# Kernel tuning notes

Measured on AMD Instinct MI355X. Metric: run time of the kernel, lower is better.

The kernel has to match this reference:

```python
import jax, jax.numpy as jnp
import numpy as np
from jax import lax

K_SQ = 8  # scaling-and-squaring steps (GridExp default)


def lrelu(x):
    return jnp.where(x >= 0, x, 0.2 * x)


def conv(x, w, b, stride=1):
    y = lax.conv_general_dilated(x, w, (stride,) * 3, 'SAME',
                                 dimension_numbers=('NCDHW', 'OIDHW', 'NCDHW'))
    return y + b[None, :, None, None, None]


def convt(x, w, b):
    y = lax.conv_transpose(x, w, (2, 2, 2), 'SAME',
                           dimension_numbers=('NCDHW', 'OIDHW', 'NCDHW'))
    return y + b[None, :, None, None, None]


def identity_grid(shape):
    rng = [jnp.arange(s, dtype=jnp.float32) for s in shape]
    return jnp.stack(jnp.meshgrid(*rng, indexing='ij'), axis=-1)


def pull_one(img, grid, extrapolate):
    # img (C, X, Y, Z); grid (..., 3) in voxel coordinates; trilinear sampling
    X, Y, Z = img.shape[1:]
    g0f = jnp.floor(grid)
    w = grid - g0f
    g0 = g0f.astype(jnp.int32)
    flat = img.reshape(img.shape[0], -1)
    out = jnp.zeros(img.shape[:1] + grid.shape[:-1], img.dtype)
    for dx in (0, 1):
        for dy in (0, 1):
            for dz in (0, 1):
                ix = jnp.clip(g0[..., 0] + dx, 0, X - 1)
                iy = jnp.clip(g0[..., 1] + dy, 0, Y - 1)
                iz = jnp.clip(g0[..., 2] + dz, 0, Z - 1)
                idx = (ix * Y + iy) * Z + iz
                val = jnp.take(flat, idx.reshape(-1), axis=1).reshape(out.shape)
                wgt = ((w[..., 0] if dx else 1 - w[..., 0]) *
                       (w[..., 1] if dy else 1 - w[..., 1]) *
                       (w[..., 2] if dz else 1 - w[..., 2]))
                out = out + wgt[None] * val
    if not extrapolate:  # zero outside the field of view (GridPull extrapolate=False)
        inb = ((grid[..., 0] >= 0) & (grid[..., 0] <= X - 1) &
               (grid[..., 1] >= 0) & (grid[..., 1] <= Y - 1) &
               (grid[..., 2] >= 0) & (grid[..., 2] <= Z - 1))
        out = out * inb[None]
    return out


pull_batch = jax.vmap(pull_one, in_axes=(0, 0, None))


def resize_field(field, out_shape, value_scale):
    # field (B, X, Y, Z, D) channel-last; trilinear resize (align-centers), scale values
    in_shape = field.shape[1:-1]
    coords = identity_grid(out_shape)
    scale = jnp.array([(i - 1) / (o - 1) for i, o in zip(in_shape, out_shape)], jnp.float32)
    coords = coords * scale
    f = jnp.moveaxis(field, -1, 1)
    cb = jnp.broadcast_to(coords, (field.shape[0],) + coords.shape)
    out = pull_batch(f, cb, True)
    return jnp.moveaxis(out, 1, -1) * value_scale


def affine_basis_cso():
    # CSO in 3D: 3 translations + 3 rotations + 1 isotropic zoom -> 7 params
    B = np.zeros((7, 4, 4), np.float32)
    for i in range(3):
        B[i, i, 3] = 1.0
    for k, (i, j) in enumerate([(0, 1), (0, 2), (1, 2)]):
        B[3 + k, i, j] = 1.0
        B[3 + k, j, i] = -1.0
    for i in range(3):
        B[6, i, i] = 1.0
    return jnp.asarray(B)


def forward_core(source, target, cnn_w, cnn_b, enc_w, enc_b, up_w, up_b, dec_w, dec_b, fin_w, fin_b):
    x = jnp.concatenate([source, target], axis=1)  # (B, 2, X, Y, Z)
    # ---- affine head CNN: 4 strided convs + head conv + global reduction -> (B, 7)
    h = x
    for i in range(4):
        h = lrelu(conv(h, cnn_w[i], cnn_b[i], stride=2))
    h = conv(h, cnn_w[4], cnn_b[4])
    aff_prm = h.mean(axis=(2, 3, 4))
    # ---- UNet velocity head -> (B, X, Y, Z, 3)
    skips = [x]
    h = x
    for i in range(4):
        h = lrelu(conv(h, enc_w[i], enc_b[i], stride=2))
        skips.append(h)
    for i in range(4):
        h = lrelu(convt(h, up_w[i], up_b[i]))
        h = jnp.concatenate([h, skips[3 - i]], axis=1)
        h = lrelu(conv(h, dec_w[i], dec_b[i]))
    vel = jnp.moveaxis(conv(h, fin_w, fin_b), 1, -1)
    shape = vel.shape[1:-1]
    small = tuple(s // 2 for s in shape)
    # ---- exp(): downsample velocity (displacement: values scaled by 0.5)
    v_small = resize_field(vel, small, 0.5)
    idg = identity_grid(small)
    d = v_small / (2.0 ** K_SQ)
    for _ in range(K_SQ):  # scaling and squaring: d <- d + d o (id + d)
        d = d + jnp.moveaxis(pull_batch(jnp.moveaxis(d, -1, 1), idg[None] + d, True), 1, -1)
    grid = resize_field(idg[None] + d, shape, 2.0)  # grid: coords scaled by 2
    # ---- affine exponential, re-centered composition
    basis = affine_basis_cso()
    A = jax.vmap(lambda p: jax.scipy.linalg.expm(jnp.einsum('k,kij->ij', p, basis)))(aff_prm)
    shift = jnp.eye(4, dtype=jnp.float32).at[:3, 3].set(-jnp.asarray(shape, jnp.float32) / 2)
    A = jnp.linalg.solve(shift[None], A @ shift[None])  # inv(shift) @ A @ shift
    lin, off = A[:, :3, :3], A[:, :3, 3]
    grid = jnp.einsum('bij,bxyzj->bxyzi', lin, grid) + off[:, None, None, None, :]
    # ---- warp source
    deformed = pull_batch(source, grid, False)
    return deformed, vel, aff_prm


def setup_inputs() -> dict:
    key = jax.random.key(0)
    ks = iter(jax.random.split(key, 48))

    def p(shape):
        return jax.random.normal(next(ks), shape, jnp.float32) * 0.05

    d = {}
    d['source'] = jax.random.normal(next(ks), (1, 1, 96, 96, 96), jnp.float32)
    d['target'] = jax.random.normal(next(ks), (1, 1, 96, 96, 96), jnp.float32)
    for i, (o, c) in enumerate([(16, 2), (32, 16), (32, 32), (32, 32), (7, 32)]):
        d[f'cnn_w{i}'] = p((o, c, 3, 3, 3)); d[f'cnn_b{i}'] = p((o,))
    for i, (o, c) in enumerate([(16, 2), (32, 16), (32, 32), (32, 32)]):
        d[f'enc_w{i}'] = p((o, c, 3, 3, 3)); d[f'enc_b{i}'] = p((o,))
    for i, (o, c) in enumerate([(32, 32), (32, 32), (32, 32), (16, 32)]):
        d[f'up_w{i}'] = p((o, c, 3, 3, 3)); d[f'up_b{i}'] = p((o,))
    for i, (o, c) in enumerate([(32, 64), (32, 64), (32, 48), (16, 18)]):
        d[f'dec_w{i}'] = p((o, c, 3, 3, 3)); d[f'dec_b{i}'] = p((o,))
    d['fin_w'] = p((3, 16, 3, 3, 3)); d['fin_b'] = p((3,))
    return d


def reference(source, target,
              cnn_w0, cnn_b0, cnn_w1, cnn_b1, cnn_w2, cnn_b2, cnn_w3, cnn_b3, cnn_w4, cnn_b4,
              enc_w0, enc_b0, enc_w1, enc_b1, enc_w2, enc_b2, enc_w3, enc_b3,
              up_w0, up_b0, up_w1, up_b1, up_w2, up_b2, up_w3, up_b3,
              dec_w0, dec_b0, dec_w1, dec_b1, dec_w2, dec_b2, dec_w3, dec_b3,
              fin_w, fin_b):
    return forward_core(
        source, target,
        [cnn_w0, cnn_w1, cnn_w2, cnn_w3, cnn_w4], [cnn_b0, cnn_b1, cnn_b2, cnn_b3, cnn_b4],
        [enc_w0, enc_w1, enc_w2, enc_w3], [enc_b0, enc_b1, enc_b2, enc_b3],
        [up_w0, up_w1, up_w2, up_w3], [up_b0, up_b1, up_b2, up_b3],
        [dec_w0, dec_w1, dec_w2, dec_w3], [dec_b0, dec_b1, dec_b2, dec_b3],
        fin_w, fin_b)
```

## Files before the change

kernel.cpp:

```cpp
#include <hip/hip_runtime.h>

#define N96 884736
#define N48 110592
#define N24 13824
#define N12 1728
#define N6  216

typedef __attribute__((ext_vector_type(4))) short short4v;
typedef __attribute__((ext_vector_type(8))) short short8v;
typedef __attribute__((ext_vector_type(4))) float f32x4;

static __device__ __forceinline__ float lrelu_f(float x){ return x >= 0.f ? x : 0.2f*x; }
static __device__ __forceinline__ int clampi(int v,int lo,int hi){ return v<lo?lo:(v>hi?hi:v); }

static __device__ __forceinline__ short f2bf(float x){
    unsigned u = __builtin_bit_cast(unsigned, x);
    unsigned r = (u + 0x7FFFu + ((u >> 16) & 1u)) >> 16;
    return (short)r;
}

template<int OCPB, int S, bool RELU>
static __device__ __forceinline__ void conv_body(
    const float* __restrict__ in1, int C1,
    const float* __restrict__ in2, int C2,
    const float* __restrict__ w, const float* __restrict__ b,
    float* __restrict__ out, int ID, int OD,
    long out_cstride, int out_vmul, int t, int oc0)
{
    int i2 = t % OD; int r = t / OD; int i1 = r % OD; int i0 = r / OD;

    float acc[OCPB];
    #pragma unroll
    for (int j=0; j<OCPB; ++j) acc[j] = b[oc0+j];

    int zz[3], yy[3], xx[3]; bool zv[3], yv[3], xv[3];
    #pragma unroll
    for (int k=0; k<3; ++k){
        int a0 = (S==2) ? (2*i0+k) : (i0+k-1);
        int a1 = (S==2) ? (2*i1+k) : (i1+k-1);
        int a2 = (S==2) ? (2*i2+k) : (i2+k-1);
        zz[k]=a0; zv[k]=(a0>=0)&&(a0<ID);
        yy[k]=a1; yv[k]=(a1>=0)&&(a1<ID);
        xx[k]=a2; xv[k]=(a2>=0)&&(a2<ID);
    }
    const int C = C1 + C2;
    const int ID2 = ID*ID;
    const long ID3 = (long)ID2*ID;

    for (int s=0; s<2; ++s){
        const float* ip = s ? in2 : in1;
        int Cs  = s ? C2 : C1;
        int icb = s ? C1 : 0;
        if (Cs == 0) continue;
        for (int ic=0; ic<Cs; ++ic){
            const float* ipb = ip + (long)ic*ID3;
            float v[27];
            #pragma unroll
            for (int kd=0; kd<3; ++kd)
            #pragma unroll
            for (int kh=0; kh<3; ++kh)
            #pragma unroll
            for (int kw=0; kw<3; ++kw){
                bool ok = zv[kd] && yv[kh] && xv[kw];
                v[kd*9+kh*3+kw] = ok ? ipb[(long)zz[kd]*ID2 + yy[kh]*ID + xx[kw]] : 0.f;
            }
            const float* wbase = w + ((long)oc0*C + (icb+ic))*27;
            #pragma unroll
            for (int j=0; j<OCPB; ++j){
                const float* wo = wbase + (long)j*C*27;
                float sacc = 0.f;
                #pragma unroll
                for (int k=0; k<27; ++k) sacc += wo[k]*v[k];
                acc[j] += sacc;
            }
        }
    }
    #pragma unroll
    for (int j=0; j<OCPB; ++j){
        float o = RELU ? lrelu_f(acc[j]) : acc[j];
        out[(long)(oc0+j)*out_cstride + (long)t*out_vmul] = o;
    }
}

template<int OCPB, int S, bool RELU>
__global__ void conv3d_k(const float* __restrict__ in1, int C1,
                         const float* __restrict__ in2, int C2,
                         const float* __restrict__ w, const float* __restrict__ b,
                         float* __restrict__ out, int ID, int OD,
                         long out_cstride, int out_vmul)
{
    int nvox = OD*OD*OD;
    int t = blockIdx.x*blockDim.x + threadIdx.x;
    if (t >= nvox) return;
    conv_body<OCPB,S,RELU>(in1,C1,in2,C2,w,b,out,ID,OD,out_cstride,out_vmul,t,blockIdx.y*OCPB);
}

template<int OCPB, int S, bool RELU>
__global__ void conv3d_dual_k(const float* __restrict__ in1A, const float* __restrict__ in2A,
                              const float* __restrict__ in1B, const float* __restrict__ in2B,
                              int C1, int C2,
                              const float* __restrict__ wA, const float* __restrict__ bA,
                              const float* __restrict__ wB, const float* __restrict__ bB,
                              float* __restrict__ outA, float* __restrict__ outB,
                              int ID, int OD)
{
    int nvox = OD*OD*OD;
    int t = blockIdx.x*blockDim.x + threadIdx.x;
    if (t >= nvox) return;
    long nv = nvox;
    if (blockIdx.z == 0)
        conv_body<OCPB,S,RELU>(in1A,C1,in2A,C2,wA,bA,outA,ID,OD,nv,1,t,blockIdx.y*OCPB);
    else
        conv_body<OCPB,S,RELU>(in1B,C1,in2B,C2,wB,bB,outB,ID,OD,nv,1,t,blockIdx.y*OCPB);
}

__global__ void e3cl_k(const float* __restrict__ e3, short* __restrict__ cl){
    int t = blockIdx.x*blockDim.x + threadIdx.x;
    if (t >= N6) return;
    #pragma unroll
    for (int grp=0; grp<4; ++grp){
        short8v v;
        #pragma unroll
        for (int c=0;c<8;++c) v[c] = f2bf(e3[(long)(8*grp+c)*N6 + t]);
        *(short8v*)(cl + (long)t*32 + 8*grp) = v;
    }
}

__global__ void fill_e0_k(const float* __restrict__ e0, short* __restrict__ cl){
    int t = blockIdx.x*blockDim.x + threadIdx.x;
    if (t >= N48) return;
    short8v v0, v1;
    #pragma unroll
    for (int c=0;c<8;++c)  v0[c] = f2bf(e0[(long)c*N48 + t]);
    #pragma unroll
    for (int c=0;c<8;++c)  v1[c] = f2bf(e0[(long)(8+c)*N48 + t]);
    short8v z = {0,0,0,0,0,0,0,0};
    *(short8v*)(cl + (long)t*64 + 32) = v0;
    *(short8v*)(cl + (long)t*64 + 40) = v1;
    *(short8v*)(cl + (long)t*64 + 48) = z;
    *(short8v*)(cl + (long)t*64 + 56) = z;
}

template<int NV>
__global__ void fill_skip32_k(const float* __restrict__ e, short* __restrict__ cl){
    int t = blockIdx.x*blockDim.x + threadIdx.x;
    if (t >= NV) return;
    #pragma unroll
    for (int grp=0; grp<4; ++grp){
        short8v v;
        #pragma unroll
        for (int c=0;c<8;++c) v[c] = f2bf(e[(long)(8*grp+c)*NV + t]);
        *(short8v*)(cl + (long)t*64 + 32 + 8*grp) = v;
    }
}

static __device__ __forceinline__ void pack_std_d(const float* __restrict__ w, short* __restrict__ pack,
                                                  int t, int CREAL, int OCREAL){
    int kidx = t >> 6, lane = t & 63;
    int oc = lane & 15, g = lane >> 4;
    short8v f;
    #pragma unroll
    for (int j=0;j<8;++j){
        int ic = 8*g + j;
        float val = (oc < OCREAL && ic < CREAL) ? w[((long)oc*CREAL + ic)*27 + kidx] : 0.f;
        f[j] = f2bf(val);
    }
    *(short8v*)(pack + (long)t*8) = f;
}
static __device__ __forceinline__ void pack_2x2_d(const float* __restrict__ w, short* __restrict__ pack,
                                                  int t, int C){
    int lane = t & 63;
    int r = t >> 6;
    int kidx = r % 27;
    int kt = (r/27) & 1;
    int ot = r/54;
    int oc = ot*16 + (lane & 15), g = lane >> 4;
    short8v f;
    #pragma unroll
    for (int j=0;j<8;++j){
        int ic = kt*32 + 8*g + j;
        float val = (ic < C) ? w[((long)oc*C + ic)*27 + kidx] : 0.f;
        f[j] = f2bf(val);
    }
    *(short8v*)(pack + (long)t*8) = f;
}
static __device__ __forceinline__ void pack_up_d(const float* __restrict__ w, short* __restrict__ pack, int t){
    int lane = t & 63;
    int r = t >> 6;
    int kidx = r % 27;
    int ot = r/27;
    int oc = ot*16 + (lane & 15), g = lane >> 4;
    short8v f;
    #pragma unroll
    for (int j=0;j<8;++j){
        int ic = 8*g + j;
        f[j] = f2bf(w[((long)oc*32 + ic)*27 + kidx]);
    }
    *(short8v*)(pack + (long)t*8) = f;
}

__global__ void pack_all_k(const float* __restrict__ dw3, const float* __restrict__ fw,
                           const float* __restrict__ uw3,
                           const float* __restrict__ dw2, const float* __restrict__ dw1,
                           const float* __restrict__ dw0,
                           const float* __restrict__ uw2, const float* __restrict__ uw1,
                           const float* __restrict__ uw0,
                           short* __restrict__ PK3, short* __restrict__ PKF, short* __restrict__ PKU,
                           short* __restrict__ PK2, short* __restrict__ PK1, short* __restrict__ PK0,
                           short* __restrict__ PKU2, short* __restrict__ PKU1, short* __restrict__ PKU0)
{
    int t = blockIdx.x*blockDim.x + threadIdx.x;
    const int S1 = 27*64;
    const int S4 = 4*27*64;
    const int S2 = 2*27*64;
    if (t < S1){ pack_std_d(dw3, PK3, t, 18, 16); return; } t -= S1;
    if (t < S1){ pack_std_d(fw,  PKF, t, 16,  3); return; } t -= S1;
    if (t < S1){ pack_std_d(uw3, PKU, t, 32, 16); return; } t -= S1;
    if (t < S4){ pack_2x2_d(dw2, PK2, t, 48); return; } t -= S4;
    if (t < S4){ pack_2x2_d(dw1, PK1, t, 64); return; } t -= S4;
    if (t < S4){ pack_2x2_d(dw0, PK0, t, 64); return; } t -= S4;
    if (t < S2){ pack_up_d(uw2, PKU2, t); return; } t -= S2;
    if (t < S2){ pack_up_d(uw1, PKU1, t); return; } t -= S2;
    if (t < S2){ pack_up_d(uw0, PKU0, t); return; }
}

template<int CSTR, int OCREAL, bool RELU, int OMODE>
__global__ __launch_bounds__(256, 4)
void conv_mfma2_k(const short* __restrict__ cl,
                  const short* __restrict__ pack,
                  const float* __restrict__ b,
                  void* __restrict__ outp)
{
    const int D2 = 96*96;
    const short8v zero8 = {0,0,0,0,0,0,0,0};
    __shared__ short lwfr[27*64*8];
    for (int idx = threadIdx.x; idx < 27*64; idx += 256)
        *(short8v*)(lwfr + (long)idx*8) = *(const short8v*)(pack + (long)idx*8);
    __syncthreads();

    int lane = threadIdx.x & 63;
    int nb = gridDim.x;
    int bid = blockIdx.x;
    int sb = (bid & 7)*(nb >> 3) + (bid >> 3);
    int wid = sb*4 + (threadIdx.x >> 6);
    int l15 = lane & 15, g = lane >> 4;
    int xh = wid & 1;
    int rem = wid >> 1;
    int y = rem % 96;
    int z = (rem / 96)*2;
    int x0b = xh*48;

    float bias = (l15 < OCREAL) ? b[l15] : 0.f;
    f32x4 acc[2][3];
    #pragma unroll
    for (int o=0;o<2;++o)
    #pragma unroll
    for (int i=0;i<3;++i) acc[o][i] = (f32x4){bias,bias,bias,bias};

    #pragma unroll
    for (int dzr=-1; dzr<=2; ++dzr){
        int zz = z + dzr;
        bool okz = (zz>=0) && (zz<96);
        int zc = okz ? zz : z;
        #pragma unroll
        for (int dy=-1; dy<=1; ++dy){
            int yy = y+dy;
            bool okrow = okz && (yy>=0) && (yy<96);
            int yc = (yy>=0 && yy<96) ? yy : y;
            long rowb = (long)zc*D2 + (long)yc*96;
            #pragma unroll
            for (int dx=-1; dx<=1; ++dx){
                short8v a[3];
                #pragma unroll
                for (int i=0;i<3;++i){
                    int x = x0b + 16*i + l15 + dx;
                    bool okx = (x>=0) && (x<96);
                    int xc = okx ? x : (x0b + 16*i + l15);
                    a[i] = *(const short8v*)(cl + (rowb + xc)*CSTR + 8*g);
                    bool oka = okrow && ((CSTR > 16) ? okx : (okx && g < 2));
                    if (!oka) a[i] = zero8;
                }
                if (dzr >= -1 && dzr <= 1){
                    int kidx = (dzr+1)*9 + (dy+1)*3 + (dx+1);
                    short8v wfr = *(const short8v*)(lwfr + ((long)kidx*64 + lane)*8);
                    #pragma unroll
                    for (int i=0;i<3;++i)
                        acc[0][i] = __builtin_amdgcn_mfma_f32_16x16x32_bf16(a[i], wfr, acc[0][i], 0, 0, 0);
                }
                if (dzr >= 0 && dzr <= 2){
                    int kidx = (dzr)*9 + (dy+1)*3 + (dx+1);
                    short8v wfr = *(const short8v*)(lwfr + ((long)kidx*64 + lane)*8);
                    #pragma unroll
                    for (int i=0;i<3;++i)
                        acc[1][i] = __builtin_amdgcn_mfma_f32_16x16x32_bf16(a[i], wfr, acc[1][i], 0, 0, 0);
                }
            }
        }
    }

    #pragma unroll
    for (int o=0;o<2;++o){
        long vrow = (long)(z+o)*D2 + (long)y*96 + x0b;
        if (OMODE == 0){
            short* op = (short*)outp;
            #pragma unroll
            for (int i=0;i<3;++i)
            #pragma unroll
            for (int reg=0; reg<4; ++reg){
                int mr = 4*g + reg;
                float v = RELU ? lrelu_f(acc[o][i][reg]) : acc[o][i][reg];
                op[(vrow + 16*i + mr)*16 + l15] = f2bf(v);
            }
        } else {
            float* op = (float*)outp;
            if (l15 < 3){
                #pragma unroll
                for (int i=0;i<3;++i)
                #pragma unroll
                for (int reg=0; reg<4; ++reg){
                    int mr = 4*g + reg;
                    op[(vrow + 16*i + mr)*3 + l15] = acc[o][i][reg];
                }
            }
        }
    }
}

__global__ __launch_bounds__(256, 2)
void conv_mfma48_k(const short* __restrict__ cl,
                   const short* __restrict__ pack,
                   const float* __restrict__ b,
                   short* __restrict__ out)
{
    const int D2 = 48*48;
    const short8v zero8 = {0,0,0,0,0,0,0,0};
    int lane = threadIdx.x & 63;
    int nb = gridDim.x;
    int bid = blockIdx.x;
    int sb = (bid & 7)*(nb >> 3) + (bid >> 3);
    int wid = sb*4 + (threadIdx.x >> 6);
    int l15 = lane & 15, g = lane >> 4;
    int y = wid % 48, z = wid / 48;

    float bias0 = b[l15];
    float bias1 = b[16 + l15];
    f32x4 acc[2][3];
    #pragma unroll
    for (int i=0;i<3;++i){ acc[0][i] = (f32x4){bias0,bias0,bias0,bias0};
                           acc[1][i] = (f32x4){bias1,bias1,bias1,bias1}; }

    #pragma unroll
    for (int dz=-1; dz<=1; ++dz){
        int zz = z+dz;
        bool okz = (zz>=0) && (zz<48);
        int zc = okz ? zz : z;
        #pragma unroll
        for (int dy=-1; dy<=1; ++dy){
            int yy = y+dy;
            bool okzy = okz && (yy>=0) && (yy<48);
            int yc = (yy>=0 && yy<48) ? yy : y;
            long rowb = (long)zc*D2 + (long)yc*48;
            #pragma unroll
            for (int dx=-1; dx<=1; ++dx){
                int kidx = (dz+1)*9 + (dy+1)*3 + (dx+1);
                #pragma unroll
                for (int kt=0; kt<2; ++kt){
                    short8v a[3];
                    #pragma unroll
                    for (int i=0;i<3;++i){
                        int x = 16*i + l15 + dx;
                        bool okx = (x>=0) && (x<48);
                        int xc = okx ? x : (16*i + l15);
                        a[i] = *(const short8v*)(cl + ((rowb + xc)*64 + kt*32 + 8*g));
                        if (!okx) a[i] = zero8;
                    }
                    #pragma unroll
                    for (int ot=0; ot<2; ++ot){
                        short8v wfr = *(const short8v*)(pack + (((long)(ot*2+kt)*27 + kidx)*64 + lane)*8);
                        if (!okzy) wfr = zero8;
                        #pragma unroll
                        for (int i=0;i<3;++i)
                            acc[ot][i] = __builtin_amdgcn_mfma_f32_16x16x32_bf16(a[i], wfr, acc[ot][i], 0, 0, 0);
                    }
                }
            }
        }
    }

    long vrow = (long)z*D2 + (long)y*48;
    #pragma unroll
    for (int ot=0; ot<2; ++ot)
    #pragma unroll
    for (int i=0;i<3;++i)
    #pragma unroll
    for (int reg=0; reg<4; ++reg){
        int mr = 4*g + reg;
        out[(vrow + 16*i + mr)*32 + ot*16 + l15] = f2bf(lrelu_f(acc[ot][i][reg]));
    }
}

template<int D>
__global__ __launch_bounds__(256, 2)
void conv_mfmaD_k(const short* __restrict__ cl,
                  const short* __restrict__ pack,
                  const float* __restrict__ b,
                  short* __restrict__ out)
{
    const short8v zero8 = {0,0,0,0,0,0,0,0};
    int lane = threadIdx.x & 63;
    int nb = gridDim.x;
    int bid = blockIdx.x;
    int sb = ((nb & 7) == 0) ? ((bid & 7)*(nb >> 3) + (bid >> 3)) : bid;
    int wid = sb*4 + (threadIdx.x >> 6);
    int ot = wid & 1;
    int s  = wid >> 1;
    int l15 = lane & 15, g = lane >> 4;
    int vL = s*16 + l15;
    int xL = vL % D; int rL = vL/D; int yL = rL % D; int zL = rL/D;

    float bias = b[ot*16 + l15];
    f32x4 acc = {bias,bias,bias,bias};

    #pragma unroll
    for (int dz=-1; dz<=1; ++dz){
        int iz = zL+dz; bool okz = (iz>=0)&&(iz<D); int izc = okz?iz:zL;
        #pragma unroll
        for (int dy=-1; dy<=1; ++dy){
            int iy = yL+dy; bool oky = (iy>=0)&&(iy<D); int iyc = oky?iy:yL;
            #pragma unroll
            for (int dx=-1; dx<=1; ++dx){
                int ix = xL+dx; bool okx = (ix>=0)&&(ix<D); int ixc = okx?ix:xL;
                bool ok = okz && oky && okx;
                long base = (((long)izc*D + iyc)*D + ixc)*64;
                int kidx = (dz+1)*9 + (dy+1)*3 + (dx+1);
                #pragma unroll
                for (int kt=0; kt<2; ++kt){
                    short8v wfr = *(const short8v*)(pack + (((long)(ot*2+kt)*27 + kidx)*64 + lane)*8);
                    short8v a = *(const short8v*)(cl + base + kt*32 + 8*g);
                    if (!ok) a = zero8;
                    acc = __builtin_amdgcn_mfma_f32_16x16x32_bf16(a, wfr, acc, 0, 0, 0);
                }
            }
        }
    }

    #pragma unroll
    for (int reg=0; reg<4; ++reg){
        int m = 4*g + reg;
        out[(long)(s*16 + m)*32 + ot*16 + l15] = f2bf(lrelu_f(acc[reg]));
    }
}

template<int IDI, int NST>
__global__ __launch_bounds__(256, 2)
void convt_mfmaup_k(const short* __restrict__ cl,
                    const short* __restrict__ pack,
                    const float* __restrict__ b,
                    short* __restrict__ o)
{
    const int D2i = IDI*IDI;
    const int OD = 2*IDI;
    const long D2o = (long)OD*OD;
    int lane = threadIdx.x & 63;
    int nb = gridDim.x;
    int bid = blockIdx.x;
    int sb = ((nb & 7) == 0) ? ((bid & 7)*(nb >> 3) + (bid >> 3)) : bid;
    int wid = sb*4 + (threadIdx.x >> 6);
    int px = wid & 1;
    int row = wid >> 1;
    int y = row % OD, z = row / OD;
    int l15 = lane & 15, g = lane >> 4;
    int pz = z & 1, py = y & 1, hz = z >> 1, hy = y >> 1;

    float bias0 = b[l15], bias1 = b[16 + l15];
    f32x4 acc[2][NST];
    #pragma unroll
    for (int i=0;i<NST;++i){ acc[0][i] = (f32x4){bias0,bias0,bias0,bias0};
                             acc[1][i] = (f32x4){bias1,bias1,bias1,bias1}; }

    int k0s[2], izs[2], nz=0;
    if (pz){ k0s[0]=1; izs[0]=hz; nz=1; }
    else { if (hz>=1){ k0s[nz]=0; izs[nz]=hz-1; ++nz; } k0s[nz]=2; izs[nz]=hz; ++nz; }
    int k1s[2], iys[2], ny=0;
    if (py){ k1s[0]=1; iys[0]=hy; ny=1; }
    else { if (hy>=1){ k1s[ny]=0; iys[ny]=hy-1; ++ny; } k1s[ny]=2; iys[ny]=hy; ++ny; }

    for (int a=0;a<nz;++a)
    for (int c=0;c<ny;++c){
        long rowb = (long)izs[a]*D2i + (long)iys[c]*IDI;
        int kbase = k0s[a]*9 + k1s[c]*3;
        int nqx = px?1:2;
        for (int qx=0; qx<nqx; ++qx){
            int k2 = px ? 1 : 2*qx;
            int xoff = px ? 0 : (qx-1);
            short8v av[NST];
            #pragma unroll
            for (int i=0;i<NST;++i){
                int ix = 16*i + l15 + xoff;
                av[i] = (short8v){0,0,0,0,0,0,0,0};
                if (ix >= 0 && ix < IDI) av[i] = *(const short8v*)(cl + ((rowb + ix)*32 + 8*g));
            }
            #pragma unroll
            for (int ot=0; ot<2; ++ot){
                short8v wfr = *(const short8v*)(pack + (((long)ot*27 + kbase + k2)*64 + lane)*8);
                #pragma unroll
                for (int i=0;i<NST;++i)
                    acc[ot][i] = __builtin_amdgcn_mfma_f32_16x16x32_bf16(av[i], wfr, acc[ot][i], 0, 0, 0);
            }
        }
    }

    #pragma unroll
    for (int ot=0; ot<2; ++ot)
    #pragma unroll
    for (int i=0;i<NST;++i)
    #pragma unroll
    for (int reg=0; reg<4; ++reg){
        int m = 16*i + 4*g + reg;
        if (m < IDI){
            long vox = (long)z*D2o + (long)y*OD + (2*m + px);
            o[vox*64 + ot*16 + l15] = f2bf(lrelu_f(acc[ot][i][reg]));
        }
    }
}

__global__ __launch_bounds__(256, 2)
void convt_mfma96_k(const short* __restrict__ cl,
                    const short* __restrict__ pack,
                    const float* __restrict__ b,
                    const float* __restrict__ src,
                    const float* __restrict__ tgt,
                    short* __restrict__ o)
{
    const int D2i = 48*48;
    const long D2o = 96*96;
    int lane = threadIdx.x & 63;
    int nb = gridDim.x;
    int bid = blockIdx.x;
    int sb = (bid & 7)*(nb >> 3) + (bid >> 3);
    int wid = sb*4 + (threadIdx.x >> 6);
    int px = wid & 1;
    int row = wid >> 1;
    int y = row % 96, z = row / 96;
    int l15 = lane & 15, g = lane >> 4;
    int pz = z & 1, py = y & 1, hz = z >> 1, hy = y >> 1;

    float bias = b[l15];
    f32x4 acc[3];
    #pragma unroll
    for (int i=0;i<3;++i) acc[i] = (f32x4){bias,bias,bias,bias};

    int k0s[2], izs[2], nz=0;
    if (pz){ k0s[0]=1; izs[0]=hz; nz=1; }
    else { if (hz>=1){ k0s[nz]=0; izs[nz]=hz-1; ++nz; } k0s[nz]=2; izs[nz]=hz; ++nz; }
    int k1s[2], iys[2], ny=0;
    if (py){ k1s[0]=1; iys[0]=hy; ny=1; }
    else { if (hy>=1){ k1s[ny]=0; iys[ny]=hy-1; ++ny; } k1s[ny]=2; iys[ny]=hy; ++ny; }

    for (int a=0;a<nz;++a)
    for (int c=0;c<ny;++c){
        long rowb = (long)izs[a]*D2i + (long)iys[c]*48;
        int kbase = k0s[a]*9 + k1s[c]*3;
        int nqx = px?1:2;
        for (int qx=0; qx<nqx; ++qx){
            int k2 = px ? 1 : 2*qx;
            int xoff = px ? 0 : (qx-1);
            short8v wfr = *(const short8v*)(pack + ((long)(kbase+k2)*64 + lane)*8);
            #pragma unroll
            for (int i=0;i<3;++i){
                int ix = 16*i + l15 + xoff;
                short8v av = {0,0,0,0,0,0,0,0};
                if (ix >= 0) av = *(const short8v*)(cl + ((rowb + ix)*32 + 8*g));
                acc[i] = __builtin_amdgcn_mfma_f32_16x16x32_bf16(av, wfr, acc[i], 0, 0, 0);
            }
        }
    }

    #pragma unroll
    for (int i=0;i<3;++i)
    #pragma unroll
    for (int reg=0; reg<4; ++reg){
        int m = 16*i + 4*g + reg;
        long vox = (long)z*D2o + (long)y*96 + (2*m + px);
        o[vox*32 + l15] = f2bf(lrelu_f(acc[i][reg]));
        if (l15 == 0)      o[vox*32 + 16] = f2bf(src[vox]);
        else if (l15 == 1) o[vox*32 + 17] = f2bf(tgt[vox]);
        else               o[vox*32 + 16 + l15] = 0;
    }
}

static __device__ void mat4mul(const double* A, const double* B, double* C){
    for (int i=0;i<4;++i) for (int j=0;j<4;++j){
        double s=0; for (int k=0;k<4;++k) s += A[i*4+k]*B[k*4+j];
        C[i*4+j]=s;
    }
}

__global__ void affine_k(const float* __restrict__ c4, float* __restrict__ aff_out, float* __restrict__ mats){
    __shared__ float p[7];
    int t = threadIdx.x;
    if (t < 7){
        float s = 0.f;
        for (int i=0;i<N6;++i) s += c4[t*N6 + i];
        p[t] = s / (float)N6;
        aff_out[t] = p[t];
    }
    __syncthreads();
    if (t == 0){
        double M[16];
        for (int i=0;i<16;++i) M[i]=0.0;
        M[0*4+3]=p[0]; M[1*4+3]=p[1]; M[2*4+3]=p[2];
        M[0*4+1]= p[3]; M[1*4+0]=-p[3];
        M[0*4+2]= p[4]; M[2*4+0]=-p[4];
        M[1*4+2]= p[5]; M[2*4+1]=-p[5];
        M[0*4+0]+=p[6]; M[1*4+1]+=p[6]; M[2*4+2]+=p[6];
        double nrm=0.0;
        for (int i=0;i<4;++i){
            double s=0; for (int j=0;j<4;++j) s += fabs(M[i*4+j]);
            if (s>nrm) nrm=s;
        }
        int jj=0;
        while (nrm > 0.25 && jj < 40){ nrm *= 0.5; ++jj; }
        double sc = 1.0; for (int q=0;q<jj;++q) sc *= 0.5;
        double Ms[16]; for (int i=0;i<16;++i) Ms[i]=M[i]*sc;
        double E[16], T[16], Tn[16];
        for (int i=0;i<16;++i){ E[i] = (i%5==0)?1.0:0.0; T[i]=E[i]; }
        for (int k=1;k<=18;++k){
            mat4mul(T, Ms, Tn);
            double inv = 1.0/(double)k;
            for (int i=0;i<16;++i){ T[i]=Tn[i]*inv; E[i]+=T[i]; }
        }
        for (int q=0;q<jj;++q){ mat4mul(E,E,Tn); for (int i=0;i<16;++i) E[i]=Tn[i]; }
        const double tsh = -48.0;
        for (int i=0;i<3;++i){
            for (int j=0;j<3;++j) mats[i*3+j] = (float)E[i*4+j];
            double rs = (E[i*4+0] - (i==0?1.0:0.0))
                      + (E[i*4+1] - (i==1?1.0:0.0))
                      + (E[i*4+2] - (i==2?1.0:0.0));
            mats[9+i] = (float)(E[i*4+3] + rs*tsh);
        }
    }
}

static __device__ __forceinline__ void trilerp3(const float* __restrict__ f, int D,
                                                float c0, float c1, float c2, float out3[3]){
    float f0=floorf(c0), f1=floorf(c1), f2=floorf(c2);
    float w0=c0-f0, w1=c1-f1, w2=c2-f2;
    int a0=(int)f0, a1=(int)f1, a2=(int)f2;
    int i0s[2]={clampi(a0,0,D-1), clampi(a0+1,0,D-1)};
    int i1s[2]={clampi(a1,0,D-1), clampi(a1+1,0,D-1)};
    int i2s[2]={clampi(a2,0,D-1), clampi(a2+1,0,D-1)};
    float w0s[2]={1.f-w0,w0}, w1s[2]={1.f-w1,w1}, w2s[2]={1.f-w2,w2};
    out3[0]=out3[1]=out3[2]=0.f;
    #pragma unroll
    for (int dx=0;dx<2;++dx)
    #pragma unroll
    for (int dy=0;dy<2;++dy)
    #pragma unroll
    for (int dz=0;dz<2;++dz){
        float wg = w0s[dx]*w1s[dy]*w2s[dz];
        const float* pp = f + ((i0s[dx]*D + i1s[dy])*D + i2s[dz])*3;
        out3[0]+=wg*pp[0]; out3[1]+=wg*pp[1]; out3[2]+=wg*pp[2];
    }
}

static __device__ __forceinline__ float trilerp1(const float* __restrict__ f, int D,
                                                 float c0, float c1, float c2){
    float f0=floorf(c0), f1=floorf(c1), f2=floorf(c2);
    float w0=c0-f0, w1=c1-f1, w2=c2-f2;
    int a0=(int)f0, a1=(int)f1, a2=(int)f2;
    int i0s[2]={clampi(a0,0,D-1), clampi(a0+1,0,D-1)};
    int i1s[2]={clampi(a1,0,D-1), clampi(a1+1,0,D-1)};
    int i2s[2]={clampi(a2,0,D-1), clampi(a2+1,0,D-1)};
    float w0s[2]={1.f-w0,w0}, w1s[2]={1.f-w1,w1}, w2s[2]={1.f-w2,w2};
    float s=0.f;
    #pragma unroll
    for (int dx=0;dx<2;++dx)
    #pragma unroll
    for (int dy=0;dy<2;++dy)
    #pragma unroll
    for (int dz=0;dz<2;++dz){
        float wg = w0s[dx]*w1s[dy]*w2s[dz];
        s += wg * f[(i0s[dx]*D + i1s[dy])*D + i2s[dz]];
    }
    return s;
}

__global__ void resize_small_k(const float* __restrict__ vel, float* __restrict__ dA){
    int t = blockIdx.x*blockDim.x + threadIdx.x;
    if (t >= N48) return;
    int i2 = t % 48; int r = t / 48; int i1 = r % 48; int i0 = r / 48;
    const float s = 95.f/47.f;
    float o[3];
    trilerp3(vel, 96, i0*s, i1*s, i2*s, o);
    const float k = 0.5f/256.f;
    dA[t*3+0]=o[0]*k; dA[t*3+1]=o[1]*k; dA[t*3+2]=o[2]*k;
}

__global__ void sq_k(const float* __restrict__ din, float* __restrict__ dout){
    int t = blockIdx.x*blockDim.x + threadIdx.x;
    if (t >= N48) return;
    int i2 = t % 48; int r = t / 48; int i1 = r % 48; int i0 = r / 48;
    float d0=din[t*3+0], d1=din[t*3+1], d2=din[t*3+2];
    float s[3];
    trilerp3(din, 48, (float)i0+d0, (float)i1+d1, (float)i2+d2, s);
    dout[t*3+0]=d0+s[0]; dout[t*3+1]=d1+s[1]; dout[t*3+2]=d2+s[2];
}

__global__ void grid_pull_k(const float* __restrict__ dfin, const float* __restrict__ src,
                            const float* __restrict__ mats, float* __restrict__ out){
    int t = blockIdx.x*blockDim.x + threadIdx.x;
    if (t >= N96) return;
    int i2 = t % 96; int r = t / 96; int i1 = r % 96; int i0 = r / 96;
    const float sc = 47.f/95.f;
    float c0=i0*sc, c1=i1*sc, c2=i2*sc;
    float s[3];
    trilerp3(dfin, 48, c0, c1, c2, s);
    float g0 = 2.f*(c0+s[0]), g1 = 2.f*(c1+s[1]), g2 = 2.f*(c2+s[2]);
    float L00=mats[0],L01=mats[1],L02=mats[2],L10=mats[3],L11=mats[4],L12=mats[5],
          L20=mats[6],L21=mats[7],L22=mats[8],o0=mats[9],o1=mats[10],o2=mats[11];
    float gg0 = L00*g0 + L01*g1 + L02*g2 + o0;
    float gg1 = L10*g0 + L11*g1 + L12*g2 + o1;
    float gg2 = L20*g0 + L21*g1 + L22*g2 + o2;
    bool inb = (gg0>=0.f)&&(gg0<=95.f)&&(gg1>=0.f)&&(gg1<=95.f)&&(gg2>=0.f)&&(gg2<=95.f);
    float val = trilerp1(src, 96, gg0, gg1, gg2);
    out[t] = inb ? val : 0.f;
}

extern "C" void kernel_launch(void* const* d_in, const int* in_sizes, int n_in,
                              void* d_out, int out_size, void* d_ws, size_t ws_size,
                              hipStream_t stream) {
    const float* src = (const float*)d_in[0];
    const float* tgt = (const float*)d_in[1];
    const float *cw[5], *cb[5], *ew[4], *eb[4], *uw[4], *ub[4], *dw[4], *db[4];
    for (int i=0;i<5;++i){ cw[i]=(const float*)d_in[2+2*i]; cb[i]=(const float*)d_in[3+2*i]; }
    for (int i=0;i<4;++i){ ew[i]=(const float*)d_in[12+2*i]; eb[i]=(const float*)d_in[13+2*i]; }
    for (int i=0;i<4;++i){ uw[i]=(const float*)d_in[20+2*i]; ub[i]=(const float*)d_in[21+2*i]; }
    for (int i=0;i<4;++i){ dw[i]=(const float*)d_in[28+2*i]; db[i]=(const float*)d_in[29+2*i]; }
    const float* fw = (const float*)d_in[36];
    const float* fb = (const float*)d_in[37];

    float* ws = (float*)d_ws;
    const long OFF_E0 = 0;
    const long OFF_E1 = OFF_E0 + 16L*N48;
    const long OFF_E2 = OFF_E1 + 32L*N24;
    const long OFF_E3 = OFF_E2 + 32L*N12;
    const long OFF_B1 = OFF_E3 + 32L*N6;
    const long OFF_B2 = OFF_B1 + 32L*N48;
    const long OFF_CL32 = OFF_B2 + 32L*N48;
    const long OFF_CL16 = OFF_CL32 + 16L*N96;
    const long OFF_DA = OFF_CL16 + 8L*N96;
    const long OFF_DB = OFF_DA + 3L*N48;
    const long OFF_MT = OFF_DB + 3L*N48;
    const long OFF_PK3 = OFF_MT + 16;
    const long OFF_PKF = OFF_PK3 + 6912;
    const long OFF_PK2 = OFF_PKF + 6912;
    const long OFF_PKU = OFF_PK2 + 27648;
    const long OFF_PK1 = OFF_PKU + 6912;
    const long OFF_PK0 = OFF_PK1 + 27648;
    const long OFF_PKU2 = OFF_PK0 + 27648;
    const long OFF_PKU1 = OFF_PKU2 + 13824;
    const long OFF_PKU0 = OFF_PKU1 + 13824;
    const long OFF_CLD2 = OFF_PKU0 + 13824;
    const long OFF_CL64B = OFF_CLD2 + 16L*N48;
    const long OFF_CLD1 = OFF_CL64B + 32L*N24;
    const long OFF_CL64C = OFF_CLD1 + 16L*N24;
    const long OFF_CLD0 = OFF_CL64C + 32L*N12;
    const long OFF_CLE3 = OFF_CLD0 + 16L*N12;
    const long WS_TOT = OFF_CLE3 + 16L*N6;
    if (ws_size < (size_t)WS_TOT*4) return;

    float* E0 = ws + OFF_E0;
    float* E1 = ws + OFF_E1;
    float* E2 = ws + OFF_E2;
    float* E3 = ws + OFF_E3;
    float* B1 = ws + OFF_B1;
    float* B2 = ws + OFF_B2;
    short* CL32 = (short*)(ws + OFF_CL32);
    short* CL16 = (short*)(ws + OFF_CL16);
    short* CL64 = (short*)(ws + OFF_CL16);
    float* DA = ws + OFF_DA;
    float* DB = ws + OFF_DB;
    float* MT = ws + OFF_MT;
    short* PK3 = (short*)(ws + OFF_PK3);
    short* PKF = (short*)(ws + OFF_PKF);
    short* PK2 = (short*)(ws + OFF_PK2);
    short* PKU = (short*)(ws + OFF_PKU);
    short* PK1 = (short*)(ws + OFF_PK1);
    short* PK0 = (short*)(ws + OFF_PK0);
    short* PKU2 = (short*)(ws + OFF_PKU2);
    short* PKU1 = (short*)(ws + OFF_PKU1);
    short* PKU0 = (short*)(ws + OFF_PKU0);
    short* CLD2 = (short*)(ws + OFF_CLD2);
    short* CL64B = (short*)(ws + OFF_CL64B);
    short* CLD1 = (short*)(ws + OFF_CLD1);
    short* CL64C = (short*)(ws + OFF_CL64C);
    short* CLD0 = (short*)(ws + OFF_CLD0);
    short* CLE3 = (short*)(ws + OFF_CLE3);

    float* out_def = (float*)d_out;
    float* out_vel = out_def + N96;
    float* out_aff = out_vel + 3L*N96;

    auto gsz = [](int n, int b){ return (n + b - 1)/b; };

    pack_all_k<<<gsz(36288,256), 256, 0, stream>>>(dw[3], fw, uw[3], dw[2], dw[1], dw[0],
                                                   uw[2], uw[1], uw[0],
                                                   PK3, PKF, PKU, PK2, PK1, PK0,
                                                   PKU2, PKU1, PKU0);

    conv3d_dual_k< 8,2,true><<<dim3(gsz(N48,256), 2,2), 256, 0, stream>>>(src,tgt, src,tgt, 1,1, cw[0],cb[0], ew[0],eb[0], B1,E0, 96,48);
    conv3d_dual_k< 4,2,true><<<dim3(gsz(N24,256), 8,2), 256, 0, stream>>>(B1,nullptr, E0,nullptr, 16,0, cw[1],cb[1], ew[1],eb[1], B2,E1, 48,24);
    conv3d_dual_k< 2,2,true><<<dim3(gsz(N12, 64),16,2),  64, 0, stream>>>(B2,nullptr, E1,nullptr, 32,0, cw[2],cb[2], ew[2],eb[2], B1,E2, 24,12);
    conv3d_dual_k< 1,2,true><<<dim3(gsz(N6 , 64),32,2),  64, 0, stream>>>(B1,nullptr, E2,nullptr, 32,0, cw[3],cb[3], ew[3],eb[3], B2,E3, 12, 6);
    conv3d_k< 1,1,false><<<dim3(gsz(N6 , 64), 7), 64, 0, stream>>>(B2,32, nullptr, 0, cw[4], cb[4], B1, 6, 6, N6, 1);
    affine_k<<<1, 64, 0, stream>>>(B1, out_aff, MT);

    e3cl_k<<<1, 256, 0, stream>>>(E3, CLE3);

    convt_mfmaup_k<6,1><<<72, 256, 0, stream>>>(CLE3, PKU0, ub[0], CL64C);
    fill_skip32_k<N12><<<gsz(N12,256), 256, 0, stream>>>(E2, CL64C);

    conv_mfmaD_k<12><<<54, 256, 0, stream>>>(CL64C, PK0, db[0], CLD0);

    convt_mfmaup_k<12,1><<<288, 256, 0, stream>>>(CLD0, PKU1, ub[1], CL64B);
    fill_skip32_k<N24><<<gsz(N24,256), 256, 0, stream>>>(E1, CL64B);

    conv_mfmaD_k<24><<<432, 256, 0, stream>>>(CL64B, PK1, db[1], CLD1);

    convt_mfmaup_k<24,2><<<1152, 256, 0, stream>>>(CLD1, PKU2, ub[2], CL64);
    fill_e0_k<<<gsz(N48,256), 256, 0, stream>>>(E0, CL64);

    conv_mfma48_k<<<576, 256, 0, stream>>>(CL64, PK2, db[2], CLD2);

    convt_mfma96_k<<<4608, 256, 0, stream>>>(CLD2, PKU, ub[3], src, tgt, CL32);

    conv_mfma2_k<32,16,true ,0><<<2304, 256, 0, stream>>>(CL32, PK3, db[3], (void*)CL16);
    conv_mfma2_k<16, 3,false,1><<<2304, 256, 0, stream>>>(CL16, PKF, fb, (void*)out_vel);

    resize_small_k<<<gsz(N48,256), 256, 0, stream>>>(out_vel, DA);
    float* da = DA; float* dbuf = DB;
    for (int it=0; it<8; ++it){
        sq_k<<<gsz(N48,256), 256, 0, stream>>>(da, dbuf);
        float* tmp = da; da = dbuf; dbuf = tmp;
    }

    grid_pull_k<<<gsz(N96,256), 256, 0, stream>>>(da, src, MT, out_def);
}
```

Baseline: 543.4 us.

## Compute 2x4 z-y output tile per wave in 96^3 MFMA conv

```diff
diff --git a/kernel.cpp b/kernel.cpp
--- a/kernel.cpp
+++ b/kernel.cpp
@@ -225,7 +225,7 @@
 }
 
 template<int CSTR, int OCREAL, bool RELU, int OMODE>
-__global__ __launch_bounds__(256, 4)
+__global__ __launch_bounds__(256, 2)
 void conv_mfma2_k(const short* __restrict__ cl,
                   const short* __restrict__ pack,
                   const float* __restrict__ b,
@@ -246,16 +246,18 @@
     int l15 = lane & 15, g = lane >> 4;
     int xh = wid & 1;
     int rem = wid >> 1;
-    int y = rem % 96;
-    int z = (rem / 96)*2;
+    int y0 = (rem % 24)*4;
+    int z  = (rem / 24)*2;
     int x0b = xh*48;
 
     float bias = (l15 < OCREAL) ? b[l15] : 0.f;
-    f32x4 acc[2][3];
-    #pragma unroll
-    for (int o=0;o<2;++o)
-    #pragma unroll
-    for (int i=0;i<3;++i) acc[o][i] = (f32x4){bias,bias,bias,bias};
+    f32x4 acc[2][4][3];
+    #pragma unroll
+    for (int oz=0;oz<2;++oz)
+    #pragma unroll
+    for (int oy=0;oy<4;++oy)
+    #pragma unroll
+    for (int i=0;i<3;++i) acc[oz][oy][i] = (f32x4){bias,bias,bias,bias};
 
     #pragma unroll
     for (int dzr=-1; dzr<=2; ++dzr){
@@ -263,44 +265,50 @@
         bool okz = (zz>=0) && (zz<96);
         int zc = okz ? zz : z;
         #pragma unroll
-        for (int dy=-1; dy<=1; ++dy){
-            int yy = y+dy;
+        for (int dyr=-1; dyr<=4; ++dyr){
+            int yy = y0 + dyr;
             bool okrow = okz && (yy>=0) && (yy<96);
-            int yc = (yy>=0 && yy<96) ? yy : y;
+            int yc = (yy>=0 && yy<96) ? yy : y0;
             long rowb = (long)zc*D2 + (long)yc*96;
-            #pragma unroll
-            for (int dx=-1; dx<=1; ++dx){
-                short8v a[3];
+            short8v a[9];
+            #pragma unroll
+            for (int dxi=0; dxi<3; ++dxi){
                 #pragma unroll
                 for (int i=0;i<3;++i){
-                    int x = x0b + 16*i + l15 + dx;
+                    int x = x0b + 16*i + l15 + dxi - 1;
                     bool okx = (x>=0) && (x<96);
                     int xc = okx ? x : (x0b + 16*i + l15);
-                    a[i] = *(const short8v*)(cl + (rowb + xc)*CSTR + 8*g);
+                    short8v t = *(const short8v*)(cl + (rowb + xc)*CSTR + 8*g);
                     bool oka = okrow && ((CSTR > 16) ? okx : (okx && g < 2));
-                    if (!oka) a[i] = zero8;
+                    a[dxi*3+i] = oka ? t : zero8;
                 }
-                if (dzr >= -1 && dzr <= 1){
-                    int kidx = (dzr+1)*9 + (dy+1)*3 + (dx+1);
-                    short8v wfr = *(const short8v*)(lwfr + ((long)kidx*64 + lane)*8);
+            }
+            #pragma unroll
+            for (int oz=0; oz<2; ++oz){
+                const int dz = dzr - oz;
+                if (dz < -1 || dz > 1) continue;
+                #pragma unroll
+                for (int oy=0; oy<4; ++oy){
+                    const int dy = dyr - oy;
+                    if (dy < -1 || dy > 1) continue;
                     #pragma unroll
-                    for (int i=0;i<3;++i)
-                        acc[0][i] = __builtin_amdgcn_mfma_f32_16x16x32_bf16(a[i], wfr, acc[0][i], 0, 0, 0);
+                    for (int dxi=0; dxi<3; ++dxi){
+                        int kidx = (dz+1)*9 + (dy+1)*3 + dxi;
+                        short8v wfr = *(const short8v*)(lwfr + ((long)kidx*64 + lane)*8);
+                        #pragma unroll
+                        for (int i=0;i<3;++i)
+                            acc[oz][oy][i] = __builtin_amdgcn_mfma_f32_16x16x32_bf16(a[dxi*3+i], wfr, acc[oz][oy][i], 0, 0, 0);
+                    }
                 }
-                if (dzr >= 0 && dzr <= 2){
-                    int kidx = (dzr)*9 + (dy+1)*3 + (dx+1);
-                    short8v wfr = *(const short8v*)(lwfr + ((long)kidx*64 + lane)*8);
-                    #pragma unroll
-                    for (int i=0;i<3;++i)
-                        acc[1][i] = __builtin_amdgcn_mfma_f32_16x16x32_bf16(a[i], wfr, acc[1][i], 0, 0, 0);
-                }
-            }
-        }
-    }
-
-    #pragma unroll
-    for (int o=0;o<2;++o){
-        long vrow = (long)(z+o)*D2 + (long)y*96 + x0b;
+            }
+        }
+    }
+
+    #pragma unroll
+    for (int oz=0;oz<2;++oz)
+    #pragma unroll
+    for (int oy=0;oy<4;++oy){
+        long vrow = (long)(z+oz)*D2 + (long)(y0+oy)*96 + x0b;
         if (OMODE == 0){
             short* op = (short*)outp;
             #pragma unroll
@@ -308,7 +316,7 @@
             #pragma unroll
             for (int reg=0; reg<4; ++reg){
                 int mr = 4*g + reg;
-                float v = RELU ? lrelu_f(acc[o][i][reg]) : acc[o][i][reg];
+                float v = RELU ? lrelu_f(acc[oz][oy][i][reg]) : acc[oz][oy][i][reg];
                 op[(vrow + 16*i + mr)*16 + l15] = f2bf(v);
             }
         } else {
@@ -319,7 +327,7 @@
                 #pragma unroll
                 for (int reg=0; reg<4; ++reg){
                     int mr = 4*g + reg;
-                    op[(vrow + 16*i + mr)*3 + l15] = acc[o][i][reg];
+                    op[(vrow + 16*i + mr)*3 + l15] = acc[oz][oy][i][reg];
                 }
             }
         }
@@ -835,8 +843,8 @@
 
     convt_mfma96_k<<<4608, 256, 0, stream>>>(CLD2, PKU, ub[3], src, tgt, CL32);
 
-    conv_mfma2_k<32,16,true ,0><<<2304, 256, 0, stream>>>(CL32, PK3, db[3], (void*)CL16);
-    conv_mfma2_k<16, 3,false,1><<<2304, 256, 0, stream>>>(CL16, PKF, fb, (void*)out_vel);
+    conv_mfma2_k<32,16,true ,0><<<576, 256, 0, stream>>>(CL32, PK3, db[3], (void*)CL16);
+    conv_mfma2_k<16, 3,false,1><<<576, 256, 0, stream>>>(CL16, PKF, fb, (void*)out_vel);
 
     resize_small_k<<<gsz(N48,256), 256, 0, stream>>>(out_vel, DA);
     float* da = DA; float* dbuf = DB;
```

Result: slower. 590.3 us (+8.6%).
